# Performance work log

Hardware: AMD Instinct MI355X
Metric: run time of the kernel (lower is better)

Reference implementation:

```python
import jax, jax.numpy as jnp
import numpy as np

N, D, E, H, TOPK = 4096, 1024, 16, 2048, 2

def _uniform_init(key, shape):
    std = 1.0 / np.sqrt(shape[-1])
    return jax.random.uniform(key, shape, jnp.float32, -std, std)

def setup_inputs() -> dict:
    key = jax.random.key(0)
    kx, kr, k0, k1 = jax.random.split(key, 4)
    x = jax.random.normal(kx, (N, D), jnp.float32)
    # top-2 sparse routing scores, zeros elsewhere (mirrors the torch usage)
    logits = jax.random.normal(kr, (N, E), jnp.float32)
    vals, idx = jax.lax.top_k(logits, TOPK)
    scores = jax.nn.softmax(vals, axis=-1)
    routing_tensor = jnp.zeros((N, E), jnp.float32).at[jnp.arange(N)[:, None], idx].set(scores)
    # expert params: depth=2 MLP per expert (init_: uniform(-1/sqrt(fan_in_last_dim), ...))
    W0 = _uniform_init(k0, (E, D, H))   # note: torch init_ uses std=1/sqrt(last dim)
    b0 = jnp.zeros((E, H), jnp.float32)
    W1 = _uniform_init(k1, (E, H, D))
    b1 = jnp.zeros((E, D), jnp.float32)
    return {"x": x, "routing_tensor": routing_tensor, "W0": W0, "b0": b0, "W1": W1, "b1": b1}

def reference(x, routing_tensor, W0, b0, W1, b1):
    # Math-equivalent to the per-expert gather/MLP/scale/scatter-add loop:
    # out[n] = sum_e routing[n,e] * MLP_e(x[n])  (score==0 contributes zero)
    h = jax.nn.gelu(jnp.einsum('nd,edh->enh', x, W0) + b0[:, None, :], approximate=False)  # [E,N,H]
    y = jnp.einsum('enh,ehd->end', h, W1) + b1[:, None, :]                                 # [E,N,D]
    out = jnp.einsum('end,ne->nd', y, routing_tensor)                                      # [N,D]
    return out
```

## Files before the change

kernel.cpp:

```cpp
#include <hip/hip_runtime.h>
#include <hip/hip_bf16.h>
#include <math.h>

#define NTOK 4096
#define DM   1024
#define NE   16
#define HID  2048
#define NPAIR (NTOK*2)

#define BM 256
#define BN 128
#define BK 32
#define LDT 40
#define MSLOTS (NPAIR/BM + NE)

typedef __attribute__((ext_vector_type(4))) float f32x4;
typedef __attribute__((ext_vector_type(8))) short bf16x8;

__device__ __forceinline__ float gelu_exact(float v) {
    return 0.5f * v * (1.0f + erff(v * 0.70710678118654752440f));
}
__device__ __forceinline__ short f2bf(float f) {
    __hip_bfloat16 b = __float2bfloat16(f);
    return __builtin_bit_cast(short, b);
}

__global__ void k_init(float* __restrict__ out, int* __restrict__ cnt, int* __restrict__ cnt2) {
    int i = blockIdx.x * blockDim.x + threadIdx.x;
    if (i < NTOK * DM / 4) ((float4*)out)[i] = make_float4(0.f, 0.f, 0.f, 0.f);
    if (i < NE) { cnt[i] = 0; cnt2[i] = 0; }
}

__global__ void k_count(const float* __restrict__ rt, int* __restrict__ cnt) {
    int i = blockIdx.x * blockDim.x + threadIdx.x;
    if (i >= NTOK * NE) return;
    if (rt[i] > 0.0f) atomicAdd(&cnt[i & (NE - 1)], 1);
}

__global__ void k_scan(const int* __restrict__ cnt, int* __restrict__ offs, int* __restrict__ ts) {
    int o = 0, t = 0;
    for (int e = 0; e < NE; ++e) {
        offs[e] = o; ts[e] = t;
        o += cnt[e];
        t += (cnt[e] + BM - 1) / BM;
    }
    ts[NE] = t;
}

__global__ void k_fill(const float* __restrict__ rt, const int* __restrict__ offs,
                       int* __restrict__ cnt2, int* __restrict__ ptok, float* __restrict__ pscore) {
    int i = blockIdx.x * blockDim.x + threadIdx.x;
    if (i >= NTOK * NE) return;
    float s = rt[i];
    if (s > 0.0f) {
        int e = i & (NE - 1);
        int n = i >> 4;
        int slot = atomicAdd(&cnt2[e], 1);
        int pos = offs[e] + slot;
        ptok[pos] = n;
        pscore[pos] = s;
    }
}

__global__ __launch_bounds__(256, 2) void k_gemm1(
    const float* __restrict__ x, const float* __restrict__ W0, const float* __restrict__ b0,
    const int* __restrict__ cnt, const int* __restrict__ offs, const int* __restrict__ ts,
    const int* __restrict__ ptok, short* __restrict__ h)
{
    __shared__ short As[BM * LDT];
    __shared__ short Bs[BN * LDT];
    __shared__ int toks_s[BM];

    int mt = blockIdx.x;
    if (mt >= ts[NE]) return;
    int e = 0;
    while (mt >= ts[e + 1]) ++e;
    int lm = mt - ts[e];
    int row0 = offs[e] + lm * BM;
    int rowsValid = min(BM, cnt[e] - lm * BM);
    int n0 = blockIdx.y * BN;
    int tid = threadIdx.x;

    toks_s[tid] = ptok[row0 + min(tid, rowsValid - 1)];
    __syncthreads();

    const float* W0e = W0 + (size_t)e * DM * HID;
    int lane = tid & 63, wid = tid >> 6;
    int wm = wid >> 1, wn = wid & 1;
    int fr = lane & 15, fg = lane >> 4;

    int bn = tid & 63, bkq = tid >> 6;
    const float* bbase = W0e + (size_t)(bkq * 8) * HID + n0 + bn;
    int am = tid;
    const float* aptr = x + (size_t)toks_s[am] * DM;

    f32x4 acc[8][4];
#pragma unroll
    for (int i = 0; i < 8; ++i)
#pragma unroll
        for (int j = 0; j < 4; ++j) acc[i][j] = (f32x4)0.0f;

    float br0[16], br1[16];
#pragma unroll
    for (int kk = 0; kk < 8; ++kk) {
        br0[kk]     = bbase[(size_t)kk * HID];
        br0[kk + 8] = bbase[(size_t)kk * HID + 64];
    }

    auto STEP = [&](float (&brC)[16], float (&brN)[16], int kt) {
        float4 ar[8];
#pragma unroll
        for (int j = 0; j < 8; ++j) ar[j] = *(const float4*)(aptr + kt + j * 4);
        bf16x8 p0, p1;
#pragma unroll
        for (int kk = 0; kk < 8; ++kk) { p0[kk] = f2bf(brC[kk]); p1[kk] = f2bf(brC[kk + 8]); }
        *(bf16x8*)&Bs[bn * LDT + bkq * 8]        = p0;
        *(bf16x8*)&Bs[(bn + 64) * LDT + bkq * 8] = p1;
        float av[32];
#pragma unroll
        for (int j = 0; j < 8; ++j) {
            av[4 * j + 0] = ar[j].x; av[4 * j + 1] = ar[j].y;
            av[4 * j + 2] = ar[j].z; av[4 * j + 3] = ar[j].w;
        }
#pragma unroll
        for (int c = 0; c < 4; ++c) {
            bf16x8 pa;
#pragma unroll
            for (int u = 0; u < 8; ++u) pa[u] = f2bf(av[c * 8 + u]);
            *(bf16x8*)&As[am * LDT + c * 8] = pa;
        }
        __syncthreads();
        if (kt + BK < DM) {
            const float* bp = bbase + (size_t)(kt + BK) * HID;
#pragma unroll
            for (int kk = 0; kk < 8; ++kk) {
                brN[kk]     = bp[(size_t)kk * HID];
                brN[kk + 8] = bp[(size_t)kk * HID + 64];
            }
        }
        bf16x8 bfr[4];
#pragma unroll
        for (int j = 0; j < 4; ++j)
            bfr[j] = *(bf16x8*)&Bs[(wn * 64 + j * 16 + fr) * LDT + fg * 8];
#pragma unroll
        for (int i = 0; i < 8; ++i) {
            bf16x8 af = *(bf16x8*)&As[(wm * 128 + i * 16 + fr) * LDT + fg * 8];
#pragma unroll
            for (int j = 0; j < 4; ++j)
                acc[i][j] = __builtin_amdgcn_mfma_f32_16x16x32_bf16(af, bfr[j], acc[i][j], 0, 0, 0);
        }
        __syncthreads();
    };

    for (int kt = 0; kt < DM; kt += 2 * BK) {
        STEP(br0, br1, kt);
        STEP(br1, br0, kt + BK);
    }

    const float* b0e = b0 + (size_t)e * HID + n0 + wn * 64;
    float bias[4];
#pragma unroll
    for (int j = 0; j < 4; ++j) bias[j] = b0e[j * 16 + fr];
#pragma unroll
    for (int i = 0; i < 8; ++i)
#pragma unroll
        for (int r = 0; r < 4; ++r) {
            int m = wm * 128 + i * 16 + fg * 4 + r;
            if (m < rowsValid) {
                short* hrow = h + (size_t)(row0 + m) * HID + n0 + wn * 64;
#pragma unroll
                for (int j = 0; j < 4; ++j)
                    hrow[j * 16 + fr] = f2bf(gelu_exact(acc[i][j][r] + bias[j]));
            }
        }
}

__global__ __launch_bounds__(256, 2) void k_gemm2(
    const short* __restrict__ h, const float* __restrict__ W1, const float* __restrict__ b1,
    const int* __restrict__ cnt, const int* __restrict__ offs, const int* __restrict__ ts,
    const int* __restrict__ ptok, const float* __restrict__ pscore,
    float* __restrict__ out)
{
    __shared__ short As[BM * LDT];
    __shared__ short Bs[BN * LDT];
    __shared__ int toks_s[BM];
    __shared__ float scs_s[BM];

    int mt = blockIdx.x;
    if (mt >= ts[NE]) return;
    int e = 0;
    while (mt >= ts[e + 1]) ++e;
    int lm = mt - ts[e];
    int row0 = offs[e] + lm * BM;
    int rowsValid = min(BM, cnt[e] - lm * BM);
    int n0 = blockIdx.y * BN;
    int tid = threadIdx.x;

    {
        int r = min(tid, rowsValid - 1);
        toks_s[tid] = ptok[row0 + r];
        scs_s[tid]  = pscore[row0 + r];
    }
    __syncthreads();

    const float* W1e = W1 + (size_t)e * HID * DM;
    int lane = tid & 63, wid = tid >> 6;
    int wm = wid >> 1, wn = wid & 1;
    int fr = lane & 15, fg = lane >> 4;

    int bn = tid & 63, bkq = tid >> 6;
    const float* bbase = W1e + (size_t)(bkq * 8) * DM + n0 + bn;
    int am = tid;
    const short* aptr = h + (size_t)(row0 + min(am, rowsValid - 1)) * HID;

    f32x4 acc[8][4];
#pragma unroll
    for (int i = 0; i < 8; ++i)
#pragma unroll
        for (int j = 0; j < 4; ++j) acc[i][j] = (f32x4)0.0f;

    float br0[16], br1[16];
#pragma unroll
    for (int kk = 0; kk < 8; ++kk) {
        br0[kk]     = bbase[(size_t)kk * DM];
        br0[kk + 8] = bbase[(size_t)kk * DM + 64];
    }

    auto STEP = [&](float (&brC)[16], float (&brN)[16], int kt) {
        bf16x8 ha[4];
#pragma unroll
        for (int c = 0; c < 4; ++c) ha[c] = *(const bf16x8*)(aptr + kt + c * 8);
        bf16x8 p0, p1;
#pragma unroll
        for (int kk = 0; kk < 8; ++kk) { p0[kk] = f2bf(brC[kk]); p1[kk] = f2bf(brC[kk + 8]); }
        *(bf16x8*)&Bs[bn * LDT + bkq * 8]        = p0;
        *(bf16x8*)&Bs[(bn + 64) * LDT + bkq * 8] = p1;
#pragma unroll
        for (int c = 0; c < 4; ++c) *(bf16x8*)&As[am * LDT + c * 8] = ha[c];
        __syncthreads();
        if (kt + BK < HID) {
            const float* bp = bbase + (size_t)(kt + BK) * DM;
#pragma unroll
            for (int kk = 0; kk < 8; ++kk) {
                brN[kk]     = bp[(size_t)kk * DM];
                brN[kk + 8] = bp[(size_t)kk * DM + 64];
            }
        }
        bf16x8 bfr[4];
#pragma unroll
        for (int j = 0; j < 4; ++j)
            bfr[j] = *(bf16x8*)&Bs[(wn * 64 + j * 16 + fr) * LDT + fg * 8];
#pragma unroll
        for (int i = 0; i < 8; ++i) {
            bf16x8 af = *(bf16x8*)&As[(wm * 128 + i * 16 + fr) * LDT + fg * 8];
#pragma unroll
            for (int j = 0; j < 4; ++j)
                acc[i][j] = __builtin_amdgcn_mfma_f32_16x16x32_bf16(af, bfr[j], acc[i][j], 0, 0, 0);
        }
        __syncthreads();
    };

    for (int kt = 0; kt < HID; kt += 2 * BK) {
        STEP(br0, br1, kt);
        STEP(br1, br0, kt + BK);
    }

    const float* b1e = b1 + (size_t)e * DM + n0 + wn * 64;
    float bias[4];
#pragma unroll
    for (int j = 0; j < 4; ++j) bias[j] = b1e[j * 16 + fr];
#pragma unroll
    for (int i = 0; i < 8; ++i)
#pragma unroll
        for (int r = 0; r < 4; ++r) {
            int m = wm * 128 + i * 16 + fg * 4 + r;
            if (m < rowsValid) {
                float sc = scs_s[m];
                float* orow = out + (size_t)toks_s[m] * DM + n0 + wn * 64;
#pragma unroll
                for (int j = 0; j < 4; ++j)
                    atomicAdd(&orow[j * 16 + fr], sc * (acc[i][j][r] + bias[j]));
            }
        }
}

extern "C" void kernel_launch(void* const* d_in, const int* in_sizes, int n_in,
                              void* d_out, int out_size, void* d_ws, size_t ws_size,
                              hipStream_t stream) {
    const float* x  = (const float*)d_in[0];
    const float* rt = (const float*)d_in[1];
    const float* W0 = (const float*)d_in[2];
    const float* b0 = (const float*)d_in[3];
    const float* W1 = (const float*)d_in[4];
    const float* b1 = (const float*)d_in[5];
    float* out = (float*)d_out;

    char* ws = (char*)d_ws;
    int* cnt  = (int*)ws;
    int* cnt2 = cnt + 16;
    int* offs = cnt + 32;
    int* ts   = cnt + 48;
    int*   ptok   = (int*)(ws + 512);
    float* pscore = (float*)(ws + 512 + NPAIR * 4);
    short* hbuf   = (short*)(ws + (1u << 20));

    k_init<<<(NTOK * DM / 4 + 255) / 256, 256, 0, stream>>>(out, cnt, cnt2);
    k_count<<<(NTOK * NE) / 256, 256, 0, stream>>>(rt, cnt);
    k_scan<<<1, 1, 0, stream>>>(cnt, offs, ts);
    k_fill<<<(NTOK * NE) / 256, 256, 0, stream>>>(rt, offs, cnt2, ptok, pscore);

    k_gemm1<<<dim3(MSLOTS, HID / BN), 256, 0, stream>>>(x, W0, b0, cnt, offs, ts, ptok, hbuf);
    k_gemm2<<<dim3(MSLOTS, DM / BN), 256, 0, stream>>>(hbuf, W1, b1, cnt, offs, ts, ptok, pscore, out);
}
```

Before: 662.9 us.

## Halve GEMM M-tile to 128, prefetch A tiles into registers, vectorize B loads

Both expert GEMM kernels drop the M tile from 256 to 128 rows, so per-warp accumulators shrink from 8x4 to 4x4 MFMA tiles and the occupancy hint rises from 2 to 3 blocks per CU. A-operand loads now go through the same register double buffer as B, so global loads for the next k-step overlap with the MFMA work. B loads become float2 per thread covering two adjacent columns. The smaller tile should waste less padding on per-expert row counts and give more blocks for the scheduler, but W0/W1 are re-read by twice as many M tiles.

Result: slower. 691.8 us (+4.4%).

```diff
diff --git a/kernel.cpp b/kernel.cpp
--- a/kernel.cpp
+++ b/kernel.cpp
@@ -8,7 +8,7 @@
 #define HID  2048
 #define NPAIR (NTOK*2)
 
-#define BM 256
+#define BM 128
 #define BN 128
 #define BK 32
 #define LDT 40
@@ -62,7 +62,7 @@
     }
 }
 
-__global__ __launch_bounds__(256, 2) void k_gemm1(
+__global__ __launch_bounds__(256, 3) void k_gemm1(
     const float* __restrict__ x, const float* __restrict__ W0, const float* __restrict__ b0,
     const int* __restrict__ cnt, const int* __restrict__ offs, const int* __restrict__ ts,
     const int* __restrict__ ptok, short* __restrict__ h)
@@ -81,7 +81,7 @@
     int n0 = blockIdx.y * BN;
     int tid = threadIdx.x;
 
-    toks_s[tid] = ptok[row0 + min(tid, rowsValid - 1)];
+    if (tid < BM) toks_s[tid] = ptok[row0 + min(tid, rowsValid - 1)];
     __syncthreads();
 
     const float* W0e = W0 + (size_t)e * DM * HID;
@@ -89,62 +89,51 @@
     int wm = wid >> 1, wn = wid & 1;
     int fr = lane & 15, fg = lane >> 4;
 
-    int bn = tid & 63, bkq = tid >> 6;
-    const float* bbase = W0e + (size_t)(bkq * 8) * HID + n0 + bn;
-    int am = tid;
-    const float* aptr = x + (size_t)toks_s[am] * DM;
-
-    f32x4 acc[8][4];
-#pragma unroll
-    for (int i = 0; i < 8; ++i)
+    int arow = tid >> 1, ahalf = tid & 1;
+    const float* aptr = x + (size_t)toks_s[arow] * DM + ahalf * 16;
+    int n2 = (tid & 63) * 2, kq = tid >> 6;
+    const float* bptr = W0e + (size_t)(kq * 8) * HID + n0 + n2;
+
+    f32x4 acc[4][4];
+#pragma unroll
+    for (int i = 0; i < 4; ++i)
 #pragma unroll
         for (int j = 0; j < 4; ++j) acc[i][j] = (f32x4)0.0f;
 
-    float br0[16], br1[16];
-#pragma unroll
-    for (int kk = 0; kk < 8; ++kk) {
-        br0[kk]     = bbase[(size_t)kk * HID];
-        br0[kk + 8] = bbase[(size_t)kk * HID + 64];
-    }
-
-    auto STEP = [&](float (&brC)[16], float (&brN)[16], int kt) {
-        float4 ar[8];
-#pragma unroll
-        for (int j = 0; j < 8; ++j) ar[j] = *(const float4*)(aptr + kt + j * 4);
-        bf16x8 p0, p1;
-#pragma unroll
-        for (int kk = 0; kk < 8; ++kk) { p0[kk] = f2bf(brC[kk]); p1[kk] = f2bf(brC[kk + 8]); }
-        *(bf16x8*)&Bs[bn * LDT + bkq * 8]        = p0;
-        *(bf16x8*)&Bs[(bn + 64) * LDT + bkq * 8] = p1;
-        float av[32];
-#pragma unroll
-        for (int j = 0; j < 8; ++j) {
-            av[4 * j + 0] = ar[j].x; av[4 * j + 1] = ar[j].y;
-            av[4 * j + 2] = ar[j].z; av[4 * j + 3] = ar[j].w;
-        }
-#pragma unroll
-        for (int c = 0; c < 4; ++c) {
-            bf16x8 pa;
-#pragma unroll
-            for (int u = 0; u < 8; ++u) pa[u] = f2bf(av[c * 8 + u]);
-            *(bf16x8*)&As[am * LDT + c * 8] = pa;
-        }
-        __syncthreads();
-        if (kt + BK < DM) {
-            const float* bp = bbase + (size_t)(kt + BK) * HID;
-#pragma unroll
-            for (int kk = 0; kk < 8; ++kk) {
-                brN[kk]     = bp[(size_t)kk * HID];
-                brN[kk + 8] = bp[(size_t)kk * HID + 64];
-            }
-        }
+    float4 ar0[4], ar1[4];
+    float2 br0[8], br1[8];
+
+    auto LOAD = [&](float4 (&ar)[4], float2 (&br)[8], int kt) {
+#pragma unroll
+        for (int j = 0; j < 4; ++j) ar[j] = *(const float4*)(aptr + kt + j * 4);
+#pragma unroll
+        for (int s = 0; s < 8; ++s) br[s] = *(const float2*)(bptr + (size_t)(kt + s) * HID);
+    };
+
+    auto STEP = [&](float4 (&ar)[4], float2 (&br)[8],
+                    float4 (&arN)[4], float2 (&brN)[8], int kt) {
+        float av[16] = {ar[0].x, ar[0].y, ar[0].z, ar[0].w,
+                        ar[1].x, ar[1].y, ar[1].z, ar[1].w,
+                        ar[2].x, ar[2].y, ar[2].z, ar[2].w,
+                        ar[3].x, ar[3].y, ar[3].z, ar[3].w};
+        bf16x8 pa0, pa1, pb0, pb1;
+#pragma unroll
+        for (int u = 0; u < 8; ++u) { pa0[u] = f2bf(av[u]); pa1[u] = f2bf(av[u + 8]); }
+#pragma unroll
+        for (int s = 0; s < 8; ++s) { pb0[s] = f2bf(br[s].x); pb1[s] = f2bf(br[s].y); }
+        *(bf16x8*)&As[arow * LDT + ahalf * 16]     = pa0;
+        *(bf16x8*)&As[arow * LDT + ahalf * 16 + 8] = pa1;
+        *(bf16x8*)&Bs[n2 * LDT + kq * 8]       = pb0;
+        *(bf16x8*)&Bs[(n2 + 1) * LDT + kq * 8] = pb1;
+        __syncthreads();
+        if (kt + BK < DM) LOAD(arN, brN, kt + BK);
         bf16x8 bfr[4];
 #pragma unroll
         for (int j = 0; j < 4; ++j)
             bfr[j] = *(bf16x8*)&Bs[(wn * 64 + j * 16 + fr) * LDT + fg * 8];
 #pragma unroll
-        for (int i = 0; i < 8; ++i) {
-            bf16x8 af = *(bf16x8*)&As[(wm * 128 + i * 16 + fr) * LDT + fg * 8];
+        for (int i = 0; i < 4; ++i) {
+            bf16x8 af = *(bf16x8*)&As[(wm * 64 + i * 16 + fr) * LDT + fg * 8];
 #pragma unroll
             for (int j = 0; j < 4; ++j)
                 acc[i][j] = __builtin_amdgcn_mfma_f32_16x16x32_bf16(af, bfr[j], acc[i][j], 0, 0, 0);
@@ -152,9 +141,10 @@
         __syncthreads();
     };
 
+    LOAD(ar0, br0, 0);
     for (int kt = 0; kt < DM; kt += 2 * BK) {
-        STEP(br0, br1, kt);
-        STEP(br1, br0, kt + BK);
+        STEP(ar0, br0, ar1, br1, kt);
+        STEP(ar1, br1, ar0, br0, kt + BK);
     }
 
     const float* b0e = b0 + (size_t)e * HID + n0 + wn * 64;
@@ -162,10 +152,10 @@
 #pragma unroll
     for (int j = 0; j < 4; ++j) bias[j] = b0e[j * 16 + fr];
 #pragma unroll
-    for (int i = 0; i < 8; ++i)
+    for (int i = 0; i < 4; ++i)
 #pragma unroll
         for (int r = 0; r < 4; ++r) {
-            int m = wm * 128 + i * 16 + fg * 4 + r;
+            int m = wm * 64 + i * 16 + fg * 4 + r;
             if (m < rowsValid) {
                 short* hrow = h + (size_t)(row0 + m) * HID + n0 + wn * 64;
 #pragma unroll
@@ -175,7 +165,7 @@
         }
 }
 
-__global__ __launch_bounds__(256, 2) void k_gemm2(
+__global__ __launch_bounds__(256, 3) void k_gemm2(
     const short* __restrict__ h, const float* __restrict__ W1, const float* __restrict__ b1,
     const int* __restrict__ cnt, const int* __restrict__ offs, const int* __restrict__ ts,
     const int* __restrict__ ptok, const float* __restrict__ pscore,
@@ -196,7 +186,7 @@
     int n0 = blockIdx.y * BN;
     int tid = threadIdx.x;
 
-    {
+    if (tid < BM) {
         int r = min(tid, rowsValid - 1);
         toks_s[tid] = ptok[row0 + r];
         scs_s[tid]  = pscore[row0 + r];
@@ -208,51 +198,45 @@
     int wm = wid >> 1, wn = wid & 1;
     int fr = lane & 15, fg = lane >> 4;
 
-    int bn = tid & 63, bkq = tid >> 6;
-    const float* bbase = W1e + (size_t)(bkq * 8) * DM + n0 + bn;
-    int am = tid;
-    const short* aptr = h + (size_t)(row0 + min(am, rowsValid - 1)) * HID;
-
-    f32x4 acc[8][4];
-#pragma unroll
-    for (int i = 0; i < 8; ++i)
+    int arow = tid >> 1, ahalf = tid & 1;
+    const short* aptr = h + (size_t)(row0 + min(arow, rowsValid - 1)) * HID + ahalf * 16;
+    int n2 = (tid & 63) * 2, kq = tid >> 6;
+    const float* bptr = W1e + (size_t)(kq * 8) * DM + n0 + n2;
+
+    f32x4 acc[4][4];
+#pragma unroll
+    for (int i = 0; i < 4; ++i)
 #pragma unroll
         for (int j = 0; j < 4; ++j) acc[i][j] = (f32x4)0.0f;
 
-    float br0[16], br1[16];
-#pragma unroll
-    for (int kk = 0; kk < 8; ++kk) {
-        br0[kk]     = bbase[(size_t)kk * DM];
-        br0[kk + 8] = bbase[(size_t)kk * DM + 64];
-    }
-
-    auto STEP = [&](float (&brC)[16], float (&brN)[16], int kt) {
-        bf16x8 ha[4];
-#pragma unroll
-        for (int c = 0; c < 4; ++c) ha[c] = *(const bf16x8*)(aptr + kt + c * 8);
-        bf16x8 p0, p1;
-#pragma unroll
-        for (int kk = 0; kk < 8; ++kk) { p0[kk] = f2bf(brC[kk]); p1[kk] = f2bf(brC[kk + 8]); }
-        *(bf16x8*)&Bs[bn * LDT + bkq * 8]        = p0;
-        *(bf16x8*)&Bs[(bn + 64) * LDT + bkq * 8] = p1;
-#pragma unroll
-        for (int c = 0; c < 4; ++c) *(bf16x8*)&As[am * LDT + c * 8] = ha[c];
-        __syncthreads();
-        if (kt + BK < HID) {
-            const float* bp = bbase + (size_t)(kt + BK) * DM;
-#pragma unroll
-            for (int kk = 0; kk < 8; ++kk) {
-                brN[kk]     = bp[(size_t)kk * DM];
-                brN[kk + 8] = bp[(size_t)kk * DM + 64];
-            }
-        }
+    bf16x8 ha0[2], ha1[2];
+    float2 br0[8], br1[8];
+
+    auto LOAD = [&](bf16x8 (&ha)[2], float2 (&br)[8], int kt) {
+        ha[0] = *(const bf16x8*)(aptr + kt);
+        ha[1] = *(const bf16x8*)(aptr + kt + 8);
+#pragma unroll
+        for (int s = 0; s < 8; ++s) br[s] = *(const float2*)(bptr + (size_t)(kt + s) * DM);
+    };
+
+    auto STEP = [&](bf16x8 (&ha)[2], float2 (&br)[8],
+                    bf16x8 (&haN)[2], float2 (&brN)[8], int kt) {
+        bf16x8 pb0, pb1;
+#pragma unroll
+        for (int s = 0; s < 8; ++s) { pb0[s] = f2bf(br[s].x); pb1[s] = f2bf(br[s].y); }
+        *(bf16x8*)&As[arow * LDT + ahalf * 16]     = ha[0];
+        *(bf16x8*)&As[arow * LDT + ahalf * 16 + 8] = ha[1];
+        *(bf16x8*)&Bs[n2 * LDT + kq * 8]       = pb0;
+        *(bf16x8*)&Bs[(n2 + 1) * LDT + kq * 8] = pb1;
+        __syncthreads();
+        if (kt + BK < HID) LOAD(haN, brN, kt + BK);
         bf16x8 bfr[4];
 #pragma unroll
         for (int j = 0; j < 4; ++j)
             bfr[j] = *(bf16x8*)&Bs[(wn * 64 + j * 16 + fr) * LDT + fg * 8];
 #pragma unroll
-        for (int i = 0; i < 8; ++i) {
-            bf16x8 af = *(bf16x8*)&As[(wm * 128 + i * 16 + fr) * LDT + fg * 8];
+        for (int i = 0; i < 4; ++i) {
+            bf16x8 af = *(bf16x8*)&As[(wm * 64 + i * 16 + fr) * LDT + fg * 8];
 #pragma unroll
             for (int j = 0; j < 4; ++j)
                 acc[i][j] = __builtin_amdgcn_mfma_f32_16x16x32_bf16(af, bfr[j], acc[i][j], 0, 0, 0);
@@ -260,9 +244,10 @@
         __syncthreads();
     };
 
+    LOAD(ha0, br0, 0);
     for (int kt = 0; kt < HID; kt += 2 * BK) {
-        STEP(br0, br1, kt);
-        STEP(br1, br0, kt + BK);
+        STEP(ha0, br0, ha1, br1, kt);
+        STEP(ha1, br1, ha0, br0, kt + BK);
     }
 
     const float* b1e = b1 + (size_t)e * DM + n0 + wn * 64;
@@ -270,10 +255,10 @@
 #pragma unroll
     for (int j = 0; j < 4; ++j) bias[j] = b1e[j * 16 + fr];
 #pragma unroll
-    for (int i = 0; i < 8; ++i)
+    for (int i = 0; i < 4; ++i)
 #pragma unroll
         for (int r = 0; r < 4; ++r) {
-            int m = wm * 128 + i * 16 + fg * 4 + r;
+            int m = wm * 64 + i * 16 + fg * 4 + r;
             if (m < rowsValid) {
                 float sc = scs_s[m];
                 float* orow = out + (size_t)toks_s[m] * DM + n0 + wn * 64;
```
